# Optimization experiments

Measured on AMD Instinct MI355X. Metric: run time of the kernel, lower is better.

Reference implementation:

```python
import math
import jax, jax.numpy as jnp
import numpy as np

H, PQ, PV = 12, 8, 12
C_S = 384
INF, EPS = 1e5, 1e-8
SOFTPLUS_INV_1 = 0.541324854612918


def _rand_rot(key, shape):
    """Random rotation matrices via normalized quaternions, shape + (3,3)."""
    q = jax.random.normal(key, shape + (4,))
    q = q / jnp.linalg.norm(q, axis=-1, keepdims=True)
    w, x, y, z = q[..., 0], q[..., 1], q[..., 2], q[..., 3]
    R = jnp.stack([
        1 - 2 * (y * y + z * z), 2 * (x * y - w * z), 2 * (x * z + w * y),
        2 * (x * y + w * z), 1 - 2 * (x * x + z * z), 2 * (y * z - w * x),
        2 * (x * z - w * y), 2 * (y * z + w * x), 1 - 2 * (x * x + y * y),
    ], axis=-1).reshape(shape + (3, 3))
    return R


def setup_inputs() -> dict:
    key = jax.random.key(0)
    ks = jax.random.split(key, 12)
    B, N1, N2 = 2, 2048, 512
    s1 = jax.random.normal(ks[0], (B, N1, C_S), dtype=jnp.float32)
    s2 = jax.random.normal(ks[1], (B, N2, C_S), dtype=jnp.float32)
    r1_rot = _rand_rot(ks[2], (B, N1)).astype(jnp.float32)
    r2_rot = _rand_rot(ks[3], (B, N2)).astype(jnp.float32)
    r1_trans = jax.random.normal(ks[4], (B, N1, 3), dtype=jnp.float32)
    r2_trans = jax.random.normal(ks[5], (B, N2, 3), dtype=jnp.float32)
    mask1 = jnp.ones((B, N1), dtype=jnp.float32)
    mask2 = jnp.ones((B, N2), dtype=jnp.float32)
    Wq = jax.random.normal(ks[6], (C_S, H * PQ * 3), dtype=jnp.float32) / math.sqrt(C_S)
    Wkv = jax.random.normal(ks[7], (C_S, H * (PQ + PV) * 3), dtype=jnp.float32) / math.sqrt(C_S)
    head_weights = jnp.full((H,), SOFTPLUS_INV_1, dtype=jnp.float32)
    Wout = jax.random.normal(ks[8], (H * PV * 4, C_S), dtype=jnp.float32) * 0.02
    bout = jnp.zeros((C_S,), dtype=jnp.float32)
    return {"s1": s1, "s2": s2, "r1_rot": r1_rot, "r1_trans": r1_trans,
            "r2_rot": r2_rot, "r2_trans": r2_trans, "mask1": mask1, "mask2": mask2,
            "Wq": Wq, "Wkv": Wkv, "head_weights": head_weights,
            "Wout": Wout, "bout": bout}


def reference(s1, s2, r1_rot, r1_trans, r2_rot, r2_trans, mask1, mask2,
              Wq, Wkv, head_weights, Wout, bout):
    B, N1, _ = s1.shape
    N2 = s2.shape[1]

    # query points: linear -> [B,N1,3,H,PQ] (torch split/stack layout) -> local [B,N1,H,PQ,3]
    q = jnp.moveaxis((s1 @ Wq).reshape(B, N1, 3, H, PQ), 2, -1)
    # rigid apply: R x + t (global frame)
    q = jnp.einsum('bimn,bihpn->bihpm', r1_rot, q) + r1_trans[:, :, None, None, :]

    kv = jnp.moveaxis((s2 @ Wkv).reshape(B, N2, 3, H, PQ + PV), 2, -1)
    kv = jnp.einsum('bjmn,bjhpn->bjhpm', r2_rot, kv) + r2_trans[:, :, None, None, :]
    k, v = kv[..., :PQ, :], kv[..., PQ:, :]  # [B,N2,H,PQ,3], [B,N2,H,PV,3]

    # sum_p ||q_p - k_p||^2 via norm expansion (avoids [B,N1,N2,H,PQ,3] tensor)
    qn = jnp.sum(q * q, axis=(-1, -2))                     # [B,N1,H]
    kn = jnp.sum(k * k, axis=(-1, -2))                     # [B,N2,H]
    cross = jnp.einsum('bihpc,bjhpc->bijh', q, k)          # [B,N1,N2,H]
    d2 = qn[:, :, None, :] + kn[:, None, :, :] - 2.0 * cross

    hw = jax.nn.softplus(head_weights) * math.sqrt(1.0 / (3 * (PQ * 9.0 / 2)))
    att = jnp.transpose(-0.5 * d2 * hw, (0, 3, 1, 2))      # [B,H,N1,N2]
    bias = INF * (mask1[:, :, None] * mask2[:, None, :] - 1.0)
    a = jax.nn.softmax(att + bias[:, None], axis=-1)

    o = jnp.einsum('bhij,bjhpc->bihpc', a, v)              # [B,N1,H,PV,3]
    # rigid invert_apply: R^T (x - t), back into local frame of residue i
    o_loc = jnp.einsum('bimn,bihpm->bihpn', r1_rot, o - r1_trans[:, :, None, None, :])

    dists = jnp.sqrt(jnp.sum(o_loc * o_loc, axis=-1) + EPS)   # [B,N1,H,PV]
    o_flat = o_loc.reshape(B, N1, H * PV, 3)
    feats = jnp.concatenate([o_flat[..., 0], o_flat[..., 1], o_flat[..., 2],
                             dists.reshape(B, N1, H * PV)], axis=-1)
    return feats @ Wout + bout
```

## Files before the change

### kernel.cpp

```cpp
#include <hip/hip_runtime.h>
#include <math.h>

#define B_ 2
#define N1_ 2048
#define N2_ 512
#define CS_ 384
#define H_ 12
#define PQ_ 8
#define PV_ 12
#define PKV_ 20
#define CQ_ (H_*PQ_*3)
#define CKV_ (H_*PKV_*3)
#define INF_ 100000.0f
#define HW_SCALE_ 0.09622504486493764f

typedef __attribute__((ext_vector_type(8))) short bf16x8;
typedef __attribute__((ext_vector_type(4))) float f32x4;

__device__ inline unsigned short f2bf(float x) {
  unsigned u = __float_as_uint(x);
  u += 0x7fffu + ((u >> 16) & 1u);
  return (unsigned short)(u >> 16);
}

__device__ inline bf16x8 cvt8(const float* __restrict__ p) {
  float4 a = *(const float4*)p;
  float4 b = *(const float4*)(p + 4);
  bf16x8 r;
  r[0] = (short)f2bf(a.x); r[1] = (short)f2bf(a.y);
  r[2] = (short)f2bf(a.z); r[3] = (short)f2bf(a.w);
  r[4] = (short)f2bf(b.x); r[5] = (short)f2bf(b.y);
  r[6] = (short)f2bf(b.z); r[7] = (short)f2bf(b.w);
  return r;
}

#define TQ_   108
#define TKV_  276
#define TWO_  216
#define VPAD_ 72
#define KN_   12
__global__ __launch_bounds__(256) void prep_kernel(
    const float* __restrict__ Wq, const float* __restrict__ Wkv,
    const float* __restrict__ Wout,
    unsigned short* __restrict__ wqT, unsigned short* __restrict__ wkvT,
    unsigned short* __restrict__ woutT,
    unsigned short* __restrict__ vtb, float* __restrict__ kn)
{
  __shared__ float lds[32][33];
  int blk = blockIdx.x, t = threadIdx.x;
  int rr0 = t >> 5, cc = t & 31;

  const float* src = nullptr; unsigned short* dst = nullptr;
  int K = 0, N = 0, k0 = 0, n0 = 0;
  if (blk < TQ_) {
    src = Wq; dst = wqT; K = 384; N = CQ_;
    k0 = (blk % 12) * 32; n0 = (blk / 12) * 32;
  } else if (blk < TQ_ + TKV_) {
    int b2 = blk - TQ_;
    src = Wkv; dst = wkvT; K = 384; N = CKV_;
    k0 = (b2 % 12) * 32; n0 = (b2 / 12) * 32;
  } else if (blk < TQ_ + TKV_ + TWO_) {
    int b3 = blk - TQ_ - TKV_;
    src = Wout; dst = woutT; K = 576; N = CS_;
    k0 = (b3 % 18) * 32; n0 = (b3 / 18) * 32;
  } else if (blk < TQ_ + TKV_ + TWO_ + VPAD_) {
    int idx = (blk - TQ_ - TKV_ - TWO_)*256 + t;
    int f = idx * 8;
    int run = f >> 9, off = f & 511;
    int bh = run / 12, cc2 = 36 + run % 12;
    uint4 z = {0u,0u,0u,0u};
    *(uint4*)(vtb + ((size_t)bh*48 + cc2)*512 + off) = z;
    return;
  } else {
    int idx = (blk - TQ_ - TKV_ - TWO_ - VPAD_)*256 + t;
    float4 z = {0.f,0.f,0.f,0.f};
    *(float4*)(kn + (size_t)idx*4) = z;
    return;
  }

  #pragma unroll
  for (int rr = 0; rr < 4; ++rr) {
    int r = rr0 + rr*8;
    if (n0 + cc < N) lds[r][cc] = src[(size_t)(k0 + r)*N + n0 + cc];
  }
  __syncthreads();
  #pragma unroll
  for (int rr = 0; rr < 4; ++rr) {
    int r = rr0 + rr*8;
    if (n0 + r < N) dst[(size_t)(n0 + r)*K + k0 + cc] = f2bf(lds[cc][r]);
  }
}

__global__ __launch_bounds__(256) void proj_mfma(
    const float* __restrict__ s1, const float* __restrict__ s2,
    const unsigned short* __restrict__ wqT, const unsigned short* __restrict__ wkvT,
    const float* __restrict__ r1_rot, const float* __restrict__ r1_trans,
    const float* __restrict__ r2_rot, const float* __restrict__ r2_trans,
    unsigned short* __restrict__ qgb, float* __restrict__ qn,
    unsigned short* __restrict__ kgb, unsigned short* __restrict__ vtb,
    float* __restrict__ kn)
{
  int wave = threadIdx.x >> 6, lane = threadIdx.x & 63;
  int col = lane & 15, g = lane >> 4;

  if (blockIdx.x < 384) {
    int wg = blockIdx.x*4 + wave;
    int strip = wg / 6;
    int nt = wg % 6;
    int i0 = strip * 16;

    f32x4 ax = {0.f,0.f,0.f,0.f}, ay = ax, az = ax;
    const float* arow = s1 + (size_t)(i0 + col)*CS_;
    const unsigned short* bx = wqT + (size_t)((nt     )*16 + col)*CS_;
    const unsigned short* by = wqT + (size_t)((nt +  6)*16 + col)*CS_;
    const unsigned short* bz = wqT + (size_t)((nt + 12)*16 + col)*CS_;
    #pragma unroll
    for (int k = 0; k < CS_; k += 32) {
      bf16x8 a = cvt8(arow + k + g*8);
      ax = __builtin_amdgcn_mfma_f32_16x16x32_bf16(a, *(const bf16x8*)(bx + k + g*8), ax, 0,0,0);
      ay = __builtin_amdgcn_mfma_f32_16x16x32_bf16(a, *(const bf16x8*)(by + k + g*8), ay, 0,0,0);
      az = __builtin_amdgcn_mfma_f32_16x16x32_bf16(a, *(const bf16x8*)(bz + k + g*8), az, 0,0,0);
    }

    int p = nt*16 + col;
    int h = p >> 3, pq = p & 7;
    float qsum[4];
    #pragma unroll
    for (int r = 0; r < 4; ++r) {
      int row = i0 + g*4 + r;
      const float* R  = r1_rot   + (size_t)row*9;
      const float* tr = r1_trans + (size_t)row*3;
      float x = ax[r], y = ay[r], z = az[r];
      float g0 = R[0]*x + R[1]*y + R[2]*z + tr[0];
      float g1 = R[3]*x + R[4]*y + R[5]*z + tr[1];
      float g2 = R[6]*x + R[7]*y + R[8]*z + tr[2];
      int b = row >> 11, i = row & (N1_-1);
      size_t rbase = ((size_t)(b*H_ + h)*N1_ + i)*32;
      qgb[rbase + pq*3]     = f2bf(g0);
      qgb[rbase + pq*3 + 1] = f2bf(g1);
      qgb[rbase + pq*3 + 2] = f2bf(g2);
      if (pq == 7) {
        uint4 z4 = {0u,0u,0u,0u};
        *(uint4*)(qgb + rbase + 24) = z4;
      }
      qsum[r] = g0*g0 + g1*g1 + g2*g2;
    }
    #pragma unroll
    for (int r = 0; r < 4; ++r) {
      qsum[r] += __shfl_xor(qsum[r], 1);
      qsum[r] += __shfl_xor(qsum[r], 2);
      qsum[r] += __shfl_xor(qsum[r], 4);
    }
    if ((col & 7) == 0) {
      int hh = nt*2 + (col >> 3);
      #pragma unroll
      for (int r = 0; r < 4; ++r) {
        int row = i0 + g*4 + r;
        int b = row >> 11, i = row & (N1_-1);
        qn[(size_t)(b*H_ + hh)*N1_ + i] = qsum[r];
      }
    }
  } else {
    int wg = (blockIdx.x - 384)*4 + wave;
    int strip = wg / 15;
    int nt = wg % 15;
    int row0 = strip * 16;

    f32x4 ax = {0.f,0.f,0.f,0.f}, ay = ax, az = ax;
    const float* arow = s2 + (size_t)(row0 + col)*CS_;
    const unsigned short* bx = wkvT + (size_t)(nt*16       + col)*CS_;
    const unsigned short* by = wkvT + (size_t)(nt*16 + 240 + col)*CS_;
    const unsigned short* bz = wkvT + (size_t)(nt*16 + 480 + col)*CS_;
    #pragma unroll
    for (int k = 0; k < CS_; k += 32) {
      bf16x8 a = cvt8(arow + k + g*8);
      ax = __builtin_amdgcn_mfma_f32_16x16x32_bf16(a, *(const bf16x8*)(bx + k + g*8), ax, 0,0,0);
      ay = __builtin_amdgcn_mfma_f32_16x16x32_bf16(a, *(const bf16x8*)(by + k + g*8), ay, 0,0,0);
      az = __builtin_amdgcn_mfma_f32_16x16x32_bf16(a, *(const bf16x8*)(bz + k + g*8), az, 0,0,0);
    }

    int p = nt*16 + col;
    int h = p / PKV_, pp = p % PKV_;
    #pragma unroll
    for (int r = 0; r < 4; ++r) {
      int row = row0 + g*4 + r;
      const float* R  = r2_rot   + (size_t)row*9;
      const float* tr = r2_trans + (size_t)row*3;
      float x = ax[r], y = ay[r], z = az[r];
      float g0 = R[0]*x + R[1]*y + R[2]*z + tr[0];
      float g1 = R[3]*x + R[4]*y + R[5]*z + tr[1];
      float g2 = R[6]*x + R[7]*y + R[8]*z + tr[2];
      int b = row >> 9, j = row & (N2_-1);
      int bh = b*H_ + h;
      if (pp < PQ_) {
        size_t base = ((size_t)bh*N2_ + j)*32 + pp*3;
        kgb[base]   = f2bf(g0);
        kgb[base+1] = f2bf(g1);
        kgb[base+2] = f2bf(g2);
        if (pp == 0) {
          uint4 z4 = {0u,0u,0u,0u};
          *(uint4*)(kgb + ((size_t)bh*N2_ + j)*32 + 24) = z4;
        }
        atomicAdd(&kn[(size_t)bh*N2_ + j], g0*g0 + g1*g1 + g2*g2);
      } else {
        int comp = (pp - PQ_)*3;
        size_t base = ((size_t)bh*48 + comp)*512 + j;
        vtb[base]        = f2bf(g0);
        vtb[base + 512]  = f2bf(g1);
        vtb[base + 1024] = f2bf(g2);
      }
    }
  }
}

#define RSTRIDE 72
#define OSTRIDE 52
__global__ __launch_bounds__(256) void attn_kernel(
    const unsigned short* __restrict__ qgb, const float* __restrict__ qn,
    const unsigned short* __restrict__ kgb, const unsigned short* __restrict__ vtb,
    const float* __restrict__ kn, const float* __restrict__ mask1,
    const float* __restrict__ mask2, const float* __restrict__ hwts,
    const float* __restrict__ rot, const float* __restrict__ trans,
    unsigned short* __restrict__ featsb)
{
  __shared__ __align__(16) unsigned short pstrip[4][16][RSTRIDE];
  __shared__ float o_s[4][16][OSTRIDE];
  __shared__ float l_s[4][16];

  int wave = threadIdx.x >> 6;
  int lane = threadIdx.x & 63;
  int col = lane & 15, g = lane >> 4;
  int pair = wave >> 1, half = wave & 1;
  int mt = blockIdx.x*2 + pair;
  int bh = mt >> 7;
  int it = mt & 127;
  int b = bh / H_, h = bh - b*H_;

  float hw = logf(1.0f + __expf(hwts[h])) * HW_SCALE_;

  bf16x8 qa = *(const bf16x8*)(qgb + (((size_t)bh*N1_ + it*16 + col)*32 + g*8));

  float ar[4], m1r[4];
  #pragma unroll
  for (int r = 0; r < 4; ++r) {
    int ig = it*16 + g*4 + r;
    ar[r]  = fmaf(-0.5f*hw, qn[(size_t)bh*N1_ + ig], -INF_);
    m1r[r] = mask1[b*N1_ + ig] * INF_;
  }

  f32x4 ot[3];
  #pragma unroll
  for (int m = 0; m < 3; ++m) ot[m] = (f32x4){0.f,0.f,0.f,0.f};
  float l[4] = {0.f,0.f,0.f,0.f};

  const unsigned short* kbase = kgb + (size_t)bh*N2_*32;
  const unsigned short* vbase = vtb + (size_t)bh*48*512;
  const float* knp = kn + (size_t)bh*N2_;
  const float* m2p = mask2 + b*N2_;

  for (int jt = half*4; jt < half*4 + 4; ++jt) {
    int j0 = jt*64;
    #pragma unroll
    for (int nt = 0; nt < 4; ++nt) {
      int jg = j0 + nt*16 + col;
      bf16x8 kb = *(const bf16x8*)(kbase + ((size_t)jg*32 + g*8));
      f32x4 dotv = __builtin_amdgcn_mfma_f32_16x16x32_bf16(
          qa, kb, (f32x4){0.f,0.f,0.f,0.f}, 0, 0, 0);
      float bc  = -0.5f*hw*knp[jg];
      float m2c = m2p[jg];
      #pragma unroll
      for (int r = 0; r < 4; ++r) {
        float logit = fmaf(hw, dotv[r], fmaf(m1r[r], m2c, ar[r] + bc));
        float w = __expf(logit);
        l[r] += w;
        pstrip[wave][g*4 + r][nt*16 + col] = f2bf(w);
      }
    }
    #pragma unroll
    for (int ks = 0; ks < 2; ++ks) {
      bf16x8 pb = *(const bf16x8*)&pstrip[wave][col][ks*32 + g*8];
      #pragma unroll
      for (int mtv = 0; mtv < 3; ++mtv) {
        bf16x8 va = *(const bf16x8*)(vbase +
            ((size_t)(mtv*16 + col))*512 + j0 + ks*32 + g*8);
        ot[mtv] = __builtin_amdgcn_mfma_f32_16x16x32_bf16(va, pb, ot[mtv], 0, 0, 0);
      }
    }
  }

  #pragma unroll
  for (int r = 0; r < 4; ++r) {
    l[r] += __shfl_xor(l[r], 1);
    l[r] += __shfl_xor(l[r], 2);
    l[r] += __shfl_xor(l[r], 4);
    l[r] += __shfl_xor(l[r], 8);
  }
  if (col == 0) {
    #pragma unroll
    for (int r = 0; r < 4; ++r) l_s[wave][g*4 + r] = l[r];
  }
  #pragma unroll
  for (int mtv = 0; mtv < 3; ++mtv)
    #pragma unroll
    for (int r = 0; r < 4; ++r)
      o_s[wave][col][mtv*16 + g*4 + r] = ot[mtv][r];
  __syncthreads();
  if (half) return;

  float inv = 1.0f / (l_s[wave][col] + l_s[wave+1][col]);
  int ig = it*16 + col;
  int row = b*N1_ + ig;
  const float* R  = rot   + (size_t)row*9;
  const float* tr = trans + (size_t)row*3;
  float R00=R[0],R01=R[1],R02=R[2],R10=R[3],R11=R[4],R12=R[5],R20=R[6],R21=R[7],R22=R[8];
  float t0=tr[0], t1=tr[1], t2=tr[2];
  unsigned short* fb = featsb + (size_t)row*576 + h*PV_;
  #pragma unroll
  for (int p = 0; p < 3; ++p) {
    int pt = g*3 + p;
    float ox = (o_s[wave][col][pt*3+0] + o_s[wave+1][col][pt*3+0])*inv - t0;
    float oy = (o_s[wave][col][pt*3+1] + o_s[wave+1][col][pt*3+1])*inv - t1;
    float oz = (o_s[wave][col][pt*3+2] + o_s[wave+1][col][pt*3+2])*inv - t2;
    float lx = R00*ox + R10*oy + R20*oz;
    float ly = R01*ox + R11*oy + R21*oz;
    float lz = R02*ox + R12*oy + R22*oz;
    float dist = sqrtf(lx*lx + ly*ly + lz*lz + 1e-8f);
    fb[pt]       = f2bf(lx);
    fb[144 + pt] = f2bf(ly);
    fb[288 + pt] = f2bf(lz);
    fb[432 + pt] = f2bf(dist);
  }
}

__global__ __launch_bounds__(1024) void outproj_mfma(
    const unsigned short* __restrict__ featsb, const unsigned short* __restrict__ woutT,
    const float* __restrict__ bout, float* __restrict__ out)
{
  __shared__ float acc_s[8][16][48];
  int wave = threadIdx.x >> 6, lane = threadIdx.x & 63;
  int col = lane & 15, g = lane >> 4;
  int nw = wave & 7, kh = wave >> 3;
  int i0 = blockIdx.x * 16;
  int n0 = nw * 48;

  f32x4 acc[3];
  #pragma unroll
  for (int m = 0; m < 3; ++m) acc[m] = (f32x4){0.f,0.f,0.f,0.f};
  const unsigned short* arow = featsb + (size_t)(i0 + col)*576 + kh*288;
  const unsigned short* b0 = woutT + (size_t)(n0      + col)*576 + kh*288;
  const unsigned short* b1 = woutT + (size_t)(n0 + 16 + col)*576 + kh*288;
  const unsigned short* b2 = woutT + (size_t)(n0 + 32 + col)*576 + kh*288;
  #pragma unroll 3
  for (int k = 0; k < 288; k += 32) {
    bf16x8 a = *(const bf16x8*)(arow + k + g*8);
    acc[0] = __builtin_amdgcn_mfma_f32_16x16x32_bf16(a, *(const bf16x8*)(b0 + k + g*8), acc[0], 0,0,0);
    acc[1] = __builtin_amdgcn_mfma_f32_16x16x32_bf16(a, *(const bf16x8*)(b1 + k + g*8), acc[1], 0,0,0);
    acc[2] = __builtin_amdgcn_mfma_f32_16x16x32_bf16(a, *(const bf16x8*)(b2 + k + g*8), acc[2], 0,0,0);
  }
  if (kh) {
    #pragma unroll
    for (int t3 = 0; t3 < 3; ++t3)
      #pragma unroll
      for (int r = 0; r < 4; ++r)
        acc_s[nw][g*4 + r][t3*16 + col] = acc[t3][r];
  }
  __syncthreads();
  if (kh) return;
  #pragma unroll
  for (int t3 = 0; t3 < 3; ++t3) {
    int n = n0 + t3*16 + col;
    float bb = bout[n];
    #pragma unroll
    for (int r = 0; r < 4; ++r) {
      int row = i0 + g*4 + r;
      out[(size_t)row*CS_ + n] = acc[t3][r] + acc_s[nw][g*4 + r][t3*16 + col] + bb;
    }
  }
}

extern "C" void kernel_launch(void* const* d_in, const int* in_sizes, int n_in,
                              void* d_out, int out_size, void* d_ws, size_t ws_size,
                              hipStream_t stream) {
  const float* s1       = (const float*)d_in[0];
  const float* s2       = (const float*)d_in[1];
  const float* r1_rot   = (const float*)d_in[2];
  const float* r1_trans = (const float*)d_in[3];
  const float* r2_rot   = (const float*)d_in[4];
  const float* r2_trans = (const float*)d_in[5];
  const float* mask1    = (const float*)d_in[6];
  const float* mask2    = (const float*)d_in[7];
  const float* Wq       = (const float*)d_in[8];
  const float* Wkv      = (const float*)d_in[9];
  const float* hwts     = (const float*)d_in[10];
  const float* Wout     = (const float*)d_in[11];
  const float* bout     = (const float*)d_in[12];
  float* out = (float*)d_out;

  float* qn = (float*)d_ws;
  float* kn = qn + (size_t)B_*H_*N1_;
  unsigned short* featsb = (unsigned short*)(kn + (size_t)B_*H_*N2_);
  unsigned short* qgb  = featsb + (size_t)B_*N1_*576;
  unsigned short* kgb  = qgb  + (size_t)B_*H_*N1_*32;
  unsigned short* vtb  = kgb  + (size_t)B_*H_*N2_*32;
  unsigned short* wqT  = vtb  + (size_t)B_*H_*48*512;
  unsigned short* wkvT = wqT  + (size_t)CQ_*CS_;
  unsigned short* woutT= wkvT + (size_t)CKV_*CS_;

  prep_kernel<<<TQ_+TKV_+TWO_+VPAD_+KN_, 256, 0, stream>>>(
      Wq, Wkv, Wout, wqT, wkvT, woutT, vtb, kn);
  proj_mfma<<<624, 256, 0, stream>>>(s1, s2, wqT, wkvT, r1_rot, r1_trans,
                                     r2_rot, r2_trans, qgb, qn, kgb, vtb, kn);
  attn_kernel<<<B_*H_*(N1_/32), 256, 0, stream>>>(qgb, qn, kgb, vtb, kn, mask1, mask2,
                                                  hwts, r1_rot, r1_trans, featsb);
  outproj_mfma<<<256, 1024, 0, stream>>>(featsb, woutT, bout, out);
}
```

Measured before the change: 158.3 us.

## Split-K the projection GEMMs and split attention keys four ways per block

```diff
diff --git a/kernel.cpp b/kernel.cpp
--- a/kernel.cpp
+++ b/kernel.cpp
@@ -91,7 +91,7 @@
   }
 }
 
-__global__ __launch_bounds__(256) void proj_mfma(
+__global__ __launch_bounds__(512) void proj_mfma(
     const float* __restrict__ s1, const float* __restrict__ s2,
     const unsigned short* __restrict__ wqT, const unsigned short* __restrict__ wkvT,
     const float* __restrict__ r1_rot, const float* __restrict__ r1_trans,
@@ -100,26 +100,45 @@
     unsigned short* __restrict__ kgb, unsigned short* __restrict__ vtb,
     float* __restrict__ kn)
 {
+  __shared__ float acc_s[4][16][48];
   int wave = threadIdx.x >> 6, lane = threadIdx.x & 63;
   int col = lane & 15, g = lane >> 4;
+  int u = wave >> 1, kh = wave & 1;
+  int koff = kh * 192;
 
   if (blockIdx.x < 384) {
-    int wg = blockIdx.x*4 + wave;
+    int wg = blockIdx.x*4 + u;
     int strip = wg / 6;
     int nt = wg % 6;
     int i0 = strip * 16;
 
     f32x4 ax = {0.f,0.f,0.f,0.f}, ay = ax, az = ax;
-    const float* arow = s1 + (size_t)(i0 + col)*CS_;
-    const unsigned short* bx = wqT + (size_t)((nt     )*16 + col)*CS_;
-    const unsigned short* by = wqT + (size_t)((nt +  6)*16 + col)*CS_;
-    const unsigned short* bz = wqT + (size_t)((nt + 12)*16 + col)*CS_;
-    #pragma unroll
-    for (int k = 0; k < CS_; k += 32) {
+    const float* arow = s1 + (size_t)(i0 + col)*CS_ + koff;
+    const unsigned short* bx = wqT + (size_t)((nt     )*16 + col)*CS_ + koff;
+    const unsigned short* by = wqT + (size_t)((nt +  6)*16 + col)*CS_ + koff;
+    const unsigned short* bz = wqT + (size_t)((nt + 12)*16 + col)*CS_ + koff;
+    #pragma unroll
+    for (int k = 0; k < 192; k += 32) {
       bf16x8 a = cvt8(arow + k + g*8);
       ax = __builtin_amdgcn_mfma_f32_16x16x32_bf16(a, *(const bf16x8*)(bx + k + g*8), ax, 0,0,0);
       ay = __builtin_amdgcn_mfma_f32_16x16x32_bf16(a, *(const bf16x8*)(by + k + g*8), ay, 0,0,0);
       az = __builtin_amdgcn_mfma_f32_16x16x32_bf16(a, *(const bf16x8*)(bz + k + g*8), az, 0,0,0);
+    }
+    if (kh) {
+      #pragma unroll
+      for (int r = 0; r < 4; ++r) {
+        acc_s[u][g*4 + r][col]      = ax[r];
+        acc_s[u][g*4 + r][16 + col] = ay[r];
+        acc_s[u][g*4 + r][32 + col] = az[r];
+      }
+    }
+    __syncthreads();
+    if (kh) return;
+    #pragma unroll
+    for (int r = 0; r < 4; ++r) {
+      ax[r] += acc_s[u][g*4 + r][col];
+      ay[r] += acc_s[u][g*4 + r][16 + col];
+      az[r] += acc_s[u][g*4 + r][32 + col];
     }
 
     int p = nt*16 + col;
@@ -161,22 +180,38 @@
       }
     }
   } else {
-    int wg = (blockIdx.x - 384)*4 + wave;
+    int wg = (blockIdx.x - 384)*4 + u;
     int strip = wg / 15;
     int nt = wg % 15;
     int row0 = strip * 16;
 
     f32x4 ax = {0.f,0.f,0.f,0.f}, ay = ax, az = ax;
-    const float* arow = s2 + (size_t)(row0 + col)*CS_;
-    const unsigned short* bx = wkvT + (size_t)(nt*16       + col)*CS_;
-    const unsigned short* by = wkvT + (size_t)(nt*16 + 240 + col)*CS_;
-    const unsigned short* bz = wkvT + (size_t)(nt*16 + 480 + col)*CS_;
-    #pragma unroll
-    for (int k = 0; k < CS_; k += 32) {
+    const float* arow = s2 + (size_t)(row0 + col)*CS_ + koff;
+    const unsigned short* bx = wkvT + (size_t)(nt*16       + col)*CS_ + koff;
+    const unsigned short* by = wkvT + (size_t)(nt*16 + 240 + col)*CS_ + koff;
+    const unsigned short* bz = wkvT + (size_t)(nt*16 + 480 + col)*CS_ + koff;
+    #pragma unroll
+    for (int k = 0; k < 192; k += 32) {
       bf16x8 a = cvt8(arow + k + g*8);
       ax = __builtin_amdgcn_mfma_f32_16x16x32_bf16(a, *(const bf16x8*)(bx + k + g*8), ax, 0,0,0);
       ay = __builtin_amdgcn_mfma_f32_16x16x32_bf16(a, *(const bf16x8*)(by + k + g*8), ay, 0,0,0);
       az = __builtin_amdgcn_mfma_f32_16x16x32_bf16(a, *(const bf16x8*)(bz + k + g*8), az, 0,0,0);
+    }
+    if (kh) {
+      #pragma unroll
+      for (int r = 0; r < 4; ++r) {
+        acc_s[u][g*4 + r][col]      = ax[r];
+        acc_s[u][g*4 + r][16 + col] = ay[r];
+        acc_s[u][g*4 + r][32 + col] = az[r];
+      }
+    }
+    __syncthreads();
+    if (kh) return;
+    #pragma unroll
+    for (int r = 0; r < 4; ++r) {
+      ax[r] += acc_s[u][g*4 + r][col];
+      ay[r] += acc_s[u][g*4 + r][16 + col];
+      az[r] += acc_s[u][g*4 + r][32 + col];
     }
 
     int p = nt*16 + col;
@@ -230,8 +265,7 @@
   int wave = threadIdx.x >> 6;
   int lane = threadIdx.x & 63;
   int col = lane & 15, g = lane >> 4;
-  int pair = wave >> 1, half = wave & 1;
-  int mt = blockIdx.x*2 + pair;
+  int mt = blockIdx.x;
   int bh = mt >> 7;
   int it = mt & 127;
   int b = bh / H_, h = bh - b*H_;
@@ -258,7 +292,9 @@
   const float* knp = kn + (size_t)bh*N2_;
   const float* m2p = mask2 + b*N2_;
 
-  for (int jt = half*4; jt < half*4 + 4; ++jt) {
+  #pragma unroll
+  for (int jj = 0; jj < 2; ++jj) {
+    int jt = wave*2 + jj;
     int j0 = jt*64;
     #pragma unroll
     for (int nt = 0; nt < 4; ++nt) {
@@ -305,9 +341,9 @@
     for (int r = 0; r < 4; ++r)
       o_s[wave][col][mtv*16 + g*4 + r] = ot[mtv][r];
   __syncthreads();
-  if (half) return;
-
-  float inv = 1.0f / (l_s[wave][col] + l_s[wave+1][col]);
+  if (wave != 0) return;
+
+  float inv = 1.0f / (l_s[0][col] + l_s[1][col] + l_s[2][col] + l_s[3][col]);
   int ig = it*16 + col;
   int row = b*N1_ + ig;
   const float* R  = rot   + (size_t)row*9;
@@ -318,9 +354,12 @@
   #pragma unroll
   for (int p = 0; p < 3; ++p) {
     int pt = g*3 + p;
-    float ox = (o_s[wave][col][pt*3+0] + o_s[wave+1][col][pt*3+0])*inv - t0;
-    float oy = (o_s[wave][col][pt*3+1] + o_s[wave+1][col][pt*3+1])*inv - t1;
-    float oz = (o_s[wave][col][pt*3+2] + o_s[wave+1][col][pt*3+2])*inv - t2;
+    float ox = (o_s[0][col][pt*3+0] + o_s[1][col][pt*3+0] +
+                o_s[2][col][pt*3+0] + o_s[3][col][pt*3+0])*inv - t0;
+    float oy = (o_s[0][col][pt*3+1] + o_s[1][col][pt*3+1] +
+                o_s[2][col][pt*3+1] + o_s[3][col][pt*3+1])*inv - t1;
+    float oz = (o_s[0][col][pt*3+2] + o_s[1][col][pt*3+2] +
+                o_s[2][col][pt*3+2] + o_s[3][col][pt*3+2])*inv - t2;
     float lx = R00*ox + R10*oy + R20*oz;
     float ly = R01*ox + R11*oy + R21*oz;
     float lz = R02*ox + R12*oy + R22*oz;
@@ -408,9 +447,9 @@
 
   prep_kernel<<<TQ_+TKV_+TWO_+VPAD_+KN_, 256, 0, stream>>>(
       Wq, Wkv, Wout, wqT, wkvT, woutT, vtb, kn);
-  proj_mfma<<<624, 256, 0, stream>>>(s1, s2, wqT, wkvT, r1_rot, r1_trans,
+  proj_mfma<<<624, 512, 0, stream>>>(s1, s2, wqT, wkvT, r1_rot, r1_trans,
                                      r2_rot, r2_trans, qgb, qn, kgb, vtb, kn);
-  attn_kernel<<<B_*H_*(N1_/32), 256, 0, stream>>>(qgb, qn, kgb, vtb, kn, mask1, mask2,
+  attn_kernel<<<B_*H_*(N1_/16), 256, 0, stream>>>(qgb, qn, kgb, vtb, kn, mask1, mask2,
                                                   hwts, r1_rot, r1_trans, featsb);
   outproj_mfma<<<256, 1024, 0, stream>>>(featsb, woutT, bout, out);
 }
```

Result: no change. 158.9 us (+0.4%).
